# Kernel optimization log

Hardware: AMD Instinct MI355X
Metric: run time of the kernel (lower is better)

## Reference

```python
import jax, jax.numpy as jnp
import numpy as np

HIDDEN = 1024
N_HEAD = 16
HEAD_DIM = HIDDEN // N_HEAD
ROPE_THETA = 10000.0


def setup_inputs() -> dict:
    key = jax.random.key(0)
    ks = jax.random.split(key, 6)
    B, T = 4, 2048
    x = jax.random.normal(ks[0], (B, T, HIDDEN), dtype=jnp.float32)
    rnn_state = jax.random.normal(ks[1], (B, HIDDEN), dtype=jnp.float32)
    Wqkv = jax.random.normal(ks[2], (HIDDEN, 3 * HIDDEN), dtype=jnp.float32) * 0.02
    bqkv = jnp.zeros((3 * HIDDEN,), dtype=jnp.float32)
    Wproj = jax.random.normal(ks[3], (HIDDEN, HIDDEN), dtype=jnp.float32) * 0.02
    bproj = jnp.zeros((HIDDEN,), dtype=jnp.float32)
    return {"x": x, "rnn_state": rnn_state, "Wqkv": Wqkv, "bqkv": bqkv,
            "Wproj": Wproj, "bproj": bproj}


def _rope_tables(T, dtype):
    # GPT-NeoX style half-split RoPE
    inv_freq = 1.0 / (ROPE_THETA ** (jnp.arange(0, HEAD_DIM, 2, dtype=jnp.float32) / HEAD_DIM))
    freqs = jnp.arange(T, dtype=jnp.float32)[:, None] * inv_freq[None, :]  # [T, D/2]
    return jnp.cos(freqs).astype(dtype), jnp.sin(freqs).astype(dtype)


def _apply_rope(x, cos, sin):
    # x: [B, H, T, D]; cos/sin: [T, D/2]
    x1, x2 = jnp.split(x, 2, axis=-1)
    c = cos[None, None, :, :]
    s = sin[None, None, :, :]
    return jnp.concatenate([x1 * c - x2 * s, x1 * s + x2 * c], axis=-1)


def reference(x, rnn_state, Wqkv, bqkv, Wproj, bproj):
    B, T, C = x.shape
    qkv = x @ Wqkv + bqkv  # [B, T, 3C]
    q, k, v = jnp.split(qkv, 3, axis=-1)
    # split heads -> [B, H, T, D]
    def heads(t):
        return t.reshape(B, T, N_HEAD, HEAD_DIM).transpose(0, 2, 1, 3)
    q, k, v = heads(q), heads(k), heads(v)
    cos, sin = _rope_tables(T, x.dtype)
    q = _apply_rope(q, cos, sin)
    k = _apply_rope(k, cos, sin)
    scale = 1.0 / jnp.sqrt(jnp.asarray(HEAD_DIM, dtype=x.dtype))
    scores = jnp.einsum('bhtd,bhsd->bhts', q, k) * scale  # [B,H,T,T]
    # causal additive mask: 0 on/below diag, -inf above (matches torch buffer)
    causal = jnp.tril(jnp.ones((T, T), dtype=bool))
    scores = jnp.where(causal[None, None, :, :], scores, -jnp.inf)
    attn = jax.nn.softmax(scores, axis=-1)
    out = jnp.einsum('bhts,bhsd->bhtd', attn, v)  # [B,H,T,D]
    out = out.transpose(0, 2, 1, 3).reshape(B, T, C)
    output = out @ Wproj + bproj
    return (output, rnn_state)
```

## Files before the change

kernel.cpp:

```cpp
#include <hip/hip_runtime.h>
#include <cstdint>
#include <cstddef>
#include <math.h>

typedef unsigned short u16;
typedef __attribute__((ext_vector_type(8))) short short8;
typedef __attribute__((ext_vector_type(4))) float floatx4;

#define HIDDEN 1024
#define NHEAD 16
#define HD 64
#define BB 4
#define TT 2048
#define MM (BB*TT)
#define NQKV 3072
#define NEGINF (-30000.0f)

__device__ inline u16 f2bf(float f){
  union { float f; unsigned u; } v; v.f = f;
  unsigned r = v.u + 0x7FFFu + ((v.u >> 16) & 1u);
  return (u16)(r >> 16);
}
__device__ inline void load_lds16(const void* g, void* l){
  __builtin_amdgcn_global_load_lds((const __attribute__((address_space(1))) void*)g,
                                   (__attribute__((address_space(3))) void*)l,
                                   16, 0, 0);
}

__global__ void rope_tables(float* __restrict__ cosT, float* __restrict__ sinT){
  const int idx = blockIdx.x * 256 + threadIdx.x;
  const int t = idx >> 5, f = idx & 31;
  const float inv = powf(10000.0f, -(float)f * (1.0f / 32.0f));
  const float ang = (float)t * inv;
  cosT[idx] = cosf(ang);
  sinT[idx] = sinf(ang);
}

__global__ void convert_x(const float* __restrict__ in, u16* __restrict__ outp){
  const int i = (blockIdx.x * 256 + threadIdx.x) * 8;
  #pragma unroll
  for (int u = 0; u < 8; u++) outp[i + u] = f2bf(in[i + u]);
}

__global__ void transpose_f32_bf16(const float* __restrict__ in, u16* __restrict__ out,
                                   int R, int C){
  __shared__ alignas(16) u16 tile[32][33];
  const int c0 = blockIdx.x * 32, r0 = blockIdx.y * 32;
  const int tx = threadIdx.x & 31, ty = threadIdx.x >> 5;
  for (int i = ty; i < 32; i += 8)
    tile[i][tx] = f2bf(in[(size_t)(r0 + i) * C + c0 + tx]);
  __syncthreads();
  for (int i = ty; i < 32; i += 8) out[(size_t)(c0 + i) * R + r0 + tx] = tile[tx][i];
}

__global__ void gemm_qkv(const u16* __restrict__ X, const u16* __restrict__ WT,
                         const float* __restrict__ bias,
                         const float* __restrict__ ropeC, const float* __restrict__ ropeS,
                         u16* __restrict__ Qb, u16* __restrict__ Kb, u16* __restrict__ Vtg)
{
  __shared__ alignas(16) u16 As[128 * 32];
  __shared__ alignas(16) u16 Bs[128 * 32];
  const int tid = threadIdx.x;
  const int wid = tid >> 6, lane = tid & 63;
  const int quad = lane >> 4, ln = lane & 15;
  const int row0 = blockIdx.y * 128, col0 = blockIdx.x * 128;
  const int wm = (wid >> 1) * 64, wn = (wid & 1) * 64;
  floatx4 acc[4][4] = {};

  const int sr = tid >> 2, sk = (tid & 3) * 8;

  for (int kk = 0; kk < 32; ++kk){
    const int k0 = kk * 32;
    __syncthreads();
    load_lds16(&X [(size_t)(row0 + sr      ) * 1024 + k0 + sk], &As[(size_t)(tid      ) * 8]);
    load_lds16(&X [(size_t)(row0 + sr + 64 ) * 1024 + k0 + sk], &As[(size_t)(tid + 256) * 8]);
    load_lds16(&WT[(size_t)(col0 + sr      ) * 1024 + k0 + sk], &Bs[(size_t)(tid      ) * 8]);
    load_lds16(&WT[(size_t)(col0 + sr + 64 ) * 1024 + k0 + sk], &Bs[(size_t)(tid + 256) * 8]);
    __syncthreads();
    short8 a[4], b[4];
    #pragma unroll
    for (int i = 0; i < 4; i++) a[i] = *(const short8*)&As[(wm + i*16 + ln) * 32 + quad * 8];
    #pragma unroll
    for (int j = 0; j < 4; j++) b[j] = *(const short8*)&Bs[(wn + j*16 + ln) * 32 + quad * 8];
    #pragma unroll
    for (int i = 0; i < 4; i++)
      #pragma unroll
      for (int j = 0; j < 4; j++)
        acc[i][j] = __builtin_amdgcn_mfma_f32_16x16x32_bf16(a[i], b[j], acc[i][j], 0, 0, 0);
  }

  const int wcol0 = col0 + wn;
  const int which = wcol0 >> 10;
  const int h = (wcol0 & 1023) >> 6;
  float bs[4];
  #pragma unroll
  for (int j = 0; j < 4; j++) bs[j] = bias[wcol0 + j*16 + ln];

  #pragma unroll
  for (int i = 0; i < 4; i++){
    #pragma unroll
    for (int rr = 0; rr < 4; rr++){
      const int rowg = row0 + wm + i*16 + quad*4 + rr;
      const int b_ = rowg >> 11, t = rowg & 2047;
      if (which < 2){
        u16* op = (which == 0 ? Qb : Kb) + ((size_t)(b_ * NHEAD + h) * TT + t) * HD;
        #pragma unroll
        for (int j = 0; j < 2; j++){
          const int f = j*16 + ln;
          const float cs = ropeC[t * 32 + f];
          const float sn = ropeS[t * 32 + f];
          const float x1 = acc[i][j  ][rr] + bs[j  ];
          const float x2 = acc[i][j+2][rr] + bs[j+2];
          float y1 = x1 * cs - x2 * sn;
          float y2 = x1 * sn + x2 * cs;
          if (which == 0){ y1 *= 0.125f; y2 *= 0.125f; }
          op[f]      = f2bf(y1);
          op[f + 32] = f2bf(y2);
        }
      } else {
        #pragma unroll
        for (int j = 0; j < 4; j++)
          Vtg[((size_t)(b_ * NHEAD + h) * HD + j*16 + ln) * TT + t] = f2bf(acc[i][j][rr] + bs[j]);
      }
    }
  }
}

__global__ void attn(const u16* __restrict__ Qb, const u16* __restrict__ Kb,
                     const u16* __restrict__ Vtg, u16* __restrict__ AO)
{
  const int bh = blockIdx.x, tbi = 31 - (int)blockIdx.y;
  const int tid = threadIdx.x;
  const int wid = tid >> 6, lane = tid & 63;
  const int quad = lane >> 4, ln = lane & 15;

  __shared__ alignas(16) u16 Kl[64 * 72];
  __shared__ alignas(16) u16 Vt[64 * 72];
  __shared__ alignas(16) u16 Pl[4][16 * 72];

  const u16* Qh = Qb  + (size_t)bh * TT * HD;
  const u16* Kh = Kb  + (size_t)bh * TT * HD;
  const u16* Vh = Vtg + (size_t)bh * HD * TT;
  const int b_ = bh >> 4, h = bh & 15;

  const int q0 = tbi * 64 + wid * 16;

  const short8 aq0 = *(const short8*)&Qh[(size_t)(q0 + ln) * HD + quad*8];
  const short8 aq1 = *(const short8*)&Qh[(size_t)(q0 + ln) * HD + 32 + quad*8];

  floatx4 o[4] = {};
  float l_i[4] = {};

  const int nch = tbi + 1;
  for (int ch = 0; ch < nch; ++ch){
    const int key0 = ch * 64;
    __syncthreads();
    #pragma unroll
    for (int it = 0; it < 2; ++it){
      const int idx = it * 256 + tid;
      const int r = idx >> 3, c8 = (idx & 7) * 8;
      *(short8*)&Kl[r * 72 + c8] = *(const short8*)&Kh[(size_t)(key0 + r) * HD + c8];
      *(short8*)&Vt[r * 72 + c8] = *(const short8*)&Vh[(size_t)r * TT + key0 + c8];
    }
    __syncthreads();

    floatx4 s[4];
    #pragma unroll
    for (int j = 0; j < 4; j++){
      const short8 kb0 = *(const short8*)&Kl[(j*16 + ln) * 72 + quad*8];
      const short8 kb1 = *(const short8*)&Kl[(j*16 + ln) * 72 + 32 + quad*8];
      floatx4 z = {0.0f, 0.0f, 0.0f, 0.0f};
      z = __builtin_amdgcn_mfma_f32_16x16x32_bf16(aq0, kb0, z, 0, 0, 0);
      z = __builtin_amdgcn_mfma_f32_16x16x32_bf16(aq1, kb1, z, 0, 0, 0);
      s[j] = z;
    }
    if (ch == nch - 1){
      #pragma unroll
      for (int j = 0; j < 4; j++)
        #pragma unroll
        for (int rr = 0; rr < 4; rr++){
          const int key = key0 + j*16 + ln;
          const int t   = q0 + quad*4 + rr;
          if (key > t) s[j][rr] = NEGINF;
        }
    }
    #pragma unroll
    for (int j = 0; j < 4; j++)
      #pragma unroll
      for (int rr = 0; rr < 4; rr++){
        const float p = __expf(s[j][rr]);
        s[j][rr] = p;
        l_i[rr] += p;
      }
    #pragma unroll
    for (int j = 0; j < 4; j++)
      #pragma unroll
      for (int rr = 0; rr < 4; rr++)
        Pl[wid][(quad*4 + rr) * 72 + j*16 + ln] = f2bf(s[j][rr]);
    const short8 pa0 = *(const short8*)&Pl[wid][ln * 72 + quad*8];
    const short8 pa1 = *(const short8*)&Pl[wid][ln * 72 + 32 + quad*8];
    #pragma unroll
    for (int n = 0; n < 4; n++){
      const short8 vb0 = *(const short8*)&Vt[(n*16 + ln) * 72 + quad*8];
      const short8 vb1 = *(const short8*)&Vt[(n*16 + ln) * 72 + 32 + quad*8];
      o[n] = __builtin_amdgcn_mfma_f32_16x16x32_bf16(pa0, vb0, o[n], 0, 0, 0);
      o[n] = __builtin_amdgcn_mfma_f32_16x16x32_bf16(pa1, vb1, o[n], 0, 0, 0);
    }
  }

  #pragma unroll
  for (int rr = 0; rr < 4; rr++){
    float rs = l_i[rr];
    #pragma unroll
    for (int off = 1; off < 16; off <<= 1) rs += __shfl_xor(rs, off);
    l_i[rr] = rs;
  }

  #pragma unroll
  for (int n = 0; n < 4; n++)
    #pragma unroll
    for (int rr = 0; rr < 4; rr++){
      const int t = q0 + quad*4 + rr;
      const float inv_l = 1.0f / fmaxf(l_i[rr], 1e-20f);
      AO[(size_t)(b_ * TT + t) * HIDDEN + h * HD + n*16 + ln] = f2bf(o[n][rr] * inv_l);
    }
}

__global__ void gemm_proj(const u16* __restrict__ A, const u16* __restrict__ WT,
                          const float* __restrict__ bias, float* __restrict__ out)
{
  __shared__ alignas(16) u16 As[128 * 32];
  __shared__ alignas(16) u16 Bs[128 * 32];
  const int tid = threadIdx.x;
  const int wid = tid >> 6, lane = tid & 63;
  const int quad = lane >> 4, ln = lane & 15;
  const int row0 = blockIdx.y * 128, col0 = blockIdx.x * 128;
  const int wm = (wid >> 1) * 64, wn = (wid & 1) * 64;
  floatx4 acc[4][4] = {};

  const int sr = tid >> 2, sk = (tid & 3) * 8;

  for (int kk = 0; kk < 32; ++kk){
    const int k0 = kk * 32;
    __syncthreads();
    load_lds16(&A [(size_t)(row0 + sr      ) * 1024 + k0 + sk], &As[(size_t)(tid      ) * 8]);
    load_lds16(&A [(size_t)(row0 + sr + 64 ) * 1024 + k0 + sk], &As[(size_t)(tid + 256) * 8]);
    load_lds16(&WT[(size_t)(col0 + sr      ) * 1024 + k0 + sk], &Bs[(size_t)(tid      ) * 8]);
    load_lds16(&WT[(size_t)(col0 + sr + 64 ) * 1024 + k0 + sk], &Bs[(size_t)(tid + 256) * 8]);
    __syncthreads();
    short8 a[4], b[4];
    #pragma unroll
    for (int i = 0; i < 4; i++) a[i] = *(const short8*)&As[(wm + i*16 + ln) * 32 + quad * 8];
    #pragma unroll
    for (int j = 0; j < 4; j++) b[j] = *(const short8*)&Bs[(wn + j*16 + ln) * 32 + quad * 8];
    #pragma unroll
    for (int i = 0; i < 4; i++)
      #pragma unroll
      for (int j = 0; j < 4; j++)
        acc[i][j] = __builtin_amdgcn_mfma_f32_16x16x32_bf16(a[i], b[j], acc[i][j], 0, 0, 0);
  }

  float bs[4];
  #pragma unroll
  for (int j = 0; j < 4; j++) bs[j] = bias[col0 + wn + j*16 + ln];
  #pragma unroll
  for (int i = 0; i < 4; i++)
    #pragma unroll
    for (int rr = 0; rr < 4; rr++){
      const int rowg = row0 + wm + i*16 + quad*4 + rr;
      #pragma unroll
      for (int j = 0; j < 4; j++)
        out[(size_t)rowg * HIDDEN + col0 + wn + j*16 + ln] = acc[i][j][rr] + bs[j];
    }
}

__global__ void copy_tail(const float* __restrict__ rnn, float* __restrict__ out){
  const int i = blockIdx.x * 256 + threadIdx.x;
  if (i < BB * HIDDEN) out[(size_t)MM * HIDDEN + i] = rnn[i];
}

extern "C" void kernel_launch(void* const* d_in, const int* in_sizes, int n_in,
                              void* d_out, int out_size, void* d_ws, size_t ws_size,
                              hipStream_t stream)
{
  const float* x     = (const float*)d_in[0];
  const float* rnn   = (const float*)d_in[1];
  const float* Wqkv  = (const float*)d_in[2];
  const float* bqkv  = (const float*)d_in[3];
  const float* Wproj = (const float*)d_in[4];
  const float* bproj = (const float*)d_in[5];
  float* out = (float*)d_out;

  char* ws = (char*)d_ws;
  size_t off = 0;
  float* ropeC  = (float*)(ws + off); off += (size_t)TT * 32 * 4;
  float* ropeS  = (float*)(ws + off); off += (size_t)TT * 32 * 4;
  u16*   xN     = (u16*)(ws + off);   off += (size_t)MM * HIDDEN * 2;
  u16*   WqkvT  = (u16*)(ws + off);   off += (size_t)NQKV * HIDDEN * 2;
  u16*   WprojT = (u16*)(ws + off);   off += (size_t)HIDDEN * HIDDEN * 2;
  u16*   Qb     = (u16*)(ws + off);   off += (size_t)MM * HIDDEN * 2;
  u16*   Kb     = (u16*)(ws + off);   off += (size_t)MM * HIDDEN * 2;
  u16*   Vtg    = (u16*)(ws + off);   off += (size_t)MM * HIDDEN * 2;
  u16*   AO     = (u16*)(ws + off);   off += (size_t)MM * HIDDEN * 2;

  rope_tables<<<(TT * 32) / 256, 256, 0, stream>>>(ropeC, ropeS);
  convert_x<<<(MM * HIDDEN) / (256 * 8), 256, 0, stream>>>(x, xN);
  transpose_f32_bf16<<<dim3(NQKV / 32, HIDDEN / 32), 256, 0, stream>>>(Wqkv, WqkvT, HIDDEN, NQKV);
  transpose_f32_bf16<<<dim3(HIDDEN / 32, HIDDEN / 32), 256, 0, stream>>>(Wproj, WprojT, HIDDEN, HIDDEN);
  gemm_qkv<<<dim3(NQKV / 128, MM / 128), 256, 0, stream>>>(xN, WqkvT, bqkv, ropeC, ropeS, Qb, Kb, Vtg);
  attn<<<dim3(BB * NHEAD, 32), 256, 0, stream>>>(Qb, Kb, Vtg, AO);
  gemm_proj<<<dim3(HIDDEN / 128, MM / 128), 256, 0, stream>>>(AO, WprojT, bproj, out);
  copy_tail<<<(BB * HIDDEN + 255) / 256, 256, 0, stream>>>(rnn, out);
}
```

Baseline: 293.8 us.

## Double-buffer GEMM LDS tiles and register-prefetch K/V chunks in attention

Both GEMM kernels now keep two LDS buffers and issue the global-to-LDS loads for the next K slice before computing on the current one, with one barrier per iteration instead of two. The attention kernel prefetches the next 64-key K and V chunk into registers while the current chunk is processed, so global load latency can overlap with MFMA work. The cost is double the GEMM shared memory and extra registers in attention, which may lower occupancy. There is also a risk that the direct-to-LDS async loads are not waited on correctly before the barrier.

```diff
diff --git a/kernel.cpp b/kernel.cpp
--- a/kernel.cpp
+++ b/kernel.cpp
@@ -58,8 +58,8 @@
                          const float* __restrict__ ropeC, const float* __restrict__ ropeS,
                          u16* __restrict__ Qb, u16* __restrict__ Kb, u16* __restrict__ Vtg)
 {
-  __shared__ alignas(16) u16 As[128 * 32];
-  __shared__ alignas(16) u16 Bs[128 * 32];
+  __shared__ alignas(16) u16 As[2][128 * 32];
+  __shared__ alignas(16) u16 Bs[2][128 * 32];
   const int tid = threadIdx.x;
   const int wid = tid >> 6, lane = tid & 63;
   const int quad = lane >> 4, ln = lane & 15;
@@ -69,24 +69,33 @@
 
   const int sr = tid >> 2, sk = (tid & 3) * 8;
 
+  load_lds16(&X [(size_t)(row0 + sr      ) * 1024 + sk], &As[0][(size_t)(tid      ) * 8]);
+  load_lds16(&X [(size_t)(row0 + sr + 64 ) * 1024 + sk], &As[0][(size_t)(tid + 256) * 8]);
+  load_lds16(&WT[(size_t)(col0 + sr      ) * 1024 + sk], &Bs[0][(size_t)(tid      ) * 8]);
+  load_lds16(&WT[(size_t)(col0 + sr + 64 ) * 1024 + sk], &Bs[0][(size_t)(tid + 256) * 8]);
+  __syncthreads();
+
+  #pragma unroll 2
   for (int kk = 0; kk < 32; ++kk){
-    const int k0 = kk * 32;
-    __syncthreads();
-    load_lds16(&X [(size_t)(row0 + sr      ) * 1024 + k0 + sk], &As[(size_t)(tid      ) * 8]);
-    load_lds16(&X [(size_t)(row0 + sr + 64 ) * 1024 + k0 + sk], &As[(size_t)(tid + 256) * 8]);
-    load_lds16(&WT[(size_t)(col0 + sr      ) * 1024 + k0 + sk], &Bs[(size_t)(tid      ) * 8]);
-    load_lds16(&WT[(size_t)(col0 + sr + 64 ) * 1024 + k0 + sk], &Bs[(size_t)(tid + 256) * 8]);
-    __syncthreads();
+    const int cur = kk & 1;
+    if (kk < 31){
+      const int k0 = (kk + 1) * 32;
+      load_lds16(&X [(size_t)(row0 + sr      ) * 1024 + k0 + sk], &As[cur ^ 1][(size_t)(tid      ) * 8]);
+      load_lds16(&X [(size_t)(row0 + sr + 64 ) * 1024 + k0 + sk], &As[cur ^ 1][(size_t)(tid + 256) * 8]);
+      load_lds16(&WT[(size_t)(col0 + sr      ) * 1024 + k0 + sk], &Bs[cur ^ 1][(size_t)(tid      ) * 8]);
+      load_lds16(&WT[(size_t)(col0 + sr + 64 ) * 1024 + k0 + sk], &Bs[cur ^ 1][(size_t)(tid + 256) * 8]);
+    }
     short8 a[4], b[4];
     #pragma unroll
-    for (int i = 0; i < 4; i++) a[i] = *(const short8*)&As[(wm + i*16 + ln) * 32 + quad * 8];
-    #pragma unroll
-    for (int j = 0; j < 4; j++) b[j] = *(const short8*)&Bs[(wn + j*16 + ln) * 32 + quad * 8];
+    for (int i = 0; i < 4; i++) a[i] = *(const short8*)&As[cur][(wm + i*16 + ln) * 32 + quad * 8];
+    #pragma unroll
+    for (int j = 0; j < 4; j++) b[j] = *(const short8*)&Bs[cur][(wn + j*16 + ln) * 32 + quad * 8];
     #pragma unroll
     for (int i = 0; i < 4; i++)
       #pragma unroll
       for (int j = 0; j < 4; j++)
         acc[i][j] = __builtin_amdgcn_mfma_f32_16x16x32_bf16(a[i], b[j], acc[i][j], 0, 0, 0);
+    __syncthreads();
   }
 
   const int wcol0 = col0 + wn;
@@ -151,16 +160,27 @@
   floatx4 o[4] = {};
   float l_i[4] = {};
 
+  const int pr = tid >> 3, pc = (tid & 7) * 8;
+
+  short8 kpre0 = *(const short8*)&Kh[(size_t)(pr     ) * HD + pc];
+  short8 kpre1 = *(const short8*)&Kh[(size_t)(pr + 32) * HD + pc];
+  short8 vpre0 = *(const short8*)&Vh[(size_t)(pr     ) * TT + pc];
+  short8 vpre1 = *(const short8*)&Vh[(size_t)(pr + 32) * TT + pc];
+
   const int nch = tbi + 1;
   for (int ch = 0; ch < nch; ++ch){
     const int key0 = ch * 64;
     __syncthreads();
-    #pragma unroll
-    for (int it = 0; it < 2; ++it){
-      const int idx = it * 256 + tid;
-      const int r = idx >> 3, c8 = (idx & 7) * 8;
-      *(short8*)&Kl[r * 72 + c8] = *(const short8*)&Kh[(size_t)(key0 + r) * HD + c8];
-      *(short8*)&Vt[r * 72 + c8] = *(const short8*)&Vh[(size_t)r * TT + key0 + c8];
+    *(short8*)&Kl[(pr     ) * 72 + pc] = kpre0;
+    *(short8*)&Kl[(pr + 32) * 72 + pc] = kpre1;
+    *(short8*)&Vt[(pr     ) * 72 + pc] = vpre0;
+    *(short8*)&Vt[(pr + 32) * 72 + pc] = vpre1;
+    if (ch + 1 < nch){
+      const int nk0 = key0 + 64;
+      kpre0 = *(const short8*)&Kh[(size_t)(nk0 + pr     ) * HD + pc];
+      kpre1 = *(const short8*)&Kh[(size_t)(nk0 + pr + 32) * HD + pc];
+      vpre0 = *(const short8*)&Vh[(size_t)(pr     ) * TT + nk0 + pc];
+      vpre1 = *(const short8*)&Vh[(size_t)(pr + 32) * TT + nk0 + pc];
     }
     __syncthreads();
 
@@ -229,8 +249,8 @@
 __global__ void gemm_proj(const u16* __restrict__ A, const u16* __restrict__ WT,
                           const float* __restrict__ bias, float* __restrict__ out)
 {
-  __shared__ alignas(16) u16 As[128 * 32];
-  __shared__ alignas(16) u16 Bs[128 * 32];
+  __shared__ alignas(16) u16 As[2][128 * 32];
+  __shared__ alignas(16) u16 Bs[2][128 * 32];
   const int tid = threadIdx.x;
   const int wid = tid >> 6, lane = tid & 63;
   const int quad = lane >> 4, ln = lane & 15;
@@ -240,24 +260,33 @@
 
   const int sr = tid >> 2, sk = (tid & 3) * 8;
 
+  load_lds16(&A [(size_t)(row0 + sr      ) * 1024 + sk], &As[0][(size_t)(tid      ) * 8]);
+  load_lds16(&A [(size_t)(row0 + sr + 64 ) * 1024 + sk], &As[0][(size_t)(tid + 256) * 8]);
+  load_lds16(&WT[(size_t)(col0 + sr      ) * 1024 + sk], &Bs[0][(size_t)(tid      ) * 8]);
+  load_lds16(&WT[(size_t)(col0 + sr + 64 ) * 1024 + sk], &Bs[0][(size_t)(tid + 256) * 8]);
+  __syncthreads();
+
+  #pragma unroll 2
   for (int kk = 0; kk < 32; ++kk){
-    const int k0 = kk * 32;
-    __syncthreads();
-    load_lds16(&A [(size_t)(row0 + sr      ) * 1024 + k0 + sk], &As[(size_t)(tid      ) * 8]);
-    load_lds16(&A [(size_t)(row0 + sr + 64 ) * 1024 + k0 + sk], &As[(size_t)(tid + 256) * 8]);
-    load_lds16(&WT[(size_t)(col0 + sr      ) * 1024 + k0 + sk], &Bs[(size_t)(tid      ) * 8]);
-    load_lds16(&WT[(size_t)(col0 + sr + 64 ) * 1024 + k0 + sk], &Bs[(size_t)(tid + 256) * 8]);
-    __syncthreads();
+    const int cur = kk & 1;
+    if (kk < 31){
+      const int k0 = (kk + 1) * 32;
+      load_lds16(&A [(size_t)(row0 + sr      ) * 1024 + k0 + sk], &As[cur ^ 1][(size_t)(tid      ) * 8]);
+      load_lds16(&A [(size_t)(row0 + sr + 64 ) * 1024 + k0 + sk], &As[cur ^ 1][(size_t)(tid + 256) * 8]);
+      load_lds16(&WT[(size_t)(col0 + sr      ) * 1024 + k0 + sk], &Bs[cur ^ 1][(size_t)(tid      ) * 8]);
+      load_lds16(&WT[(size_t)(col0 + sr + 64 ) * 1024 + k0 + sk], &Bs[cur ^ 1][(size_t)(tid + 256) * 8]);
+    }
     short8 a[4], b[4];
     #pragma unroll
-    for (int i = 0; i < 4; i++) a[i] = *(const short8*)&As[(wm + i*16 + ln) * 32 + quad * 8];
-    #pragma unroll
-    for (int j = 0; j < 4; j++) b[j] = *(const short8*)&Bs[(wn + j*16 + ln) * 32 + quad * 8];
+    for (int i = 0; i < 4; i++) a[i] = *(const short8*)&As[cur][(wm + i*16 + ln) * 32 + quad * 8];
+    #pragma unroll
+    for (int j = 0; j < 4; j++) b[j] = *(const short8*)&Bs[cur][(wn + j*16 + ln) * 32 + quad * 8];
     #pragma unroll
     for (int i = 0; i < 4; i++)
       #pragma unroll
       for (int j = 0; j < 4; j++)
         acc[i][j] = __builtin_amdgcn_mfma_f32_16x16x32_bf16(a[i], b[j], acc[i][j], 0, 0, 0);
+    __syncthreads();
   }
 
   float bs[4];
```

Result: no change. 294.7 us (+0.3%).
